# Performance work log

Measured on AMD Instinct MI355X. Metric: run time of the kernel, lower is better.

The kernel has to match this reference:

```python
import jax, jax.numpy as jnp
import numpy as np

B, T, I = 32, 512, 1024
H, HS = 8, 128  # n_heads, head_size; hidden = H*HS = 1024
LIM = 1.0 / np.sqrt(HS)


def setup_inputs() -> dict:
    key = jax.random.key(0)
    kx, kif, kzo, khh, kb = jax.random.split(key, 5)
    u = lambda k, shp: jax.random.uniform(k, shp, jnp.float32, -LIM, LIM)
    return {
        "xs": jax.random.normal(kx, (B, T, I), jnp.float32),
        "weight_if": u(kif, (H, 2 * HS, I)),
        "weight_zo": u(kzo, (H, 2 * HS, I)),
        "weight_hh": u(khh, (H, 4 * HS, HS)),
        "bias": u(kb, (H, 4 * HS)),
    }


def reference(xs, weight_if, weight_zo, weight_hh, bias):
    # xs: [B, T, I]. Scan the sLSTM cell over time, batched over B via einsum.
    b, t, _ = xs.shape
    n_heads, four_hs, head_size = weight_hh.shape

    def step(state, x):  # x: [B, I]
        h, c, m, n = state  # each [B, H, HS]
        if_lin = jnp.einsum('hki,bi->bhk', weight_if, x)  # [B, H, 2*HS]
        zo_lin = jnp.einsum('hki,bi->bhk', weight_zo, x)  # [B, H, 2*HS]
        lin = jnp.concatenate([if_lin, zo_lin], axis=2)
        lin = lin + jnp.einsum('hkd,bhd->bhk', weight_hh, h) + bias  # [B, H, 4*HS]
        i, f, z, o = jnp.split(lin, 4, axis=2)
        z = jnp.tanh(z)
        o = jax.nn.sigmoid(o)
        m_new = jnp.maximum(f + m, i)          # stabilizer
        i_e = jnp.exp(i - m_new)
        f_e = jnp.exp(f + m - m_new)
        c_new = f_e * c + i_e * z
        n_new = f_e * n + i_e
        h_new = o * (c_new / n_new)
        return (h_new, c_new, m_new, n_new), h_new.reshape(b, n_heads * head_size)

    init = tuple(jnp.zeros((b, n_heads, head_size), xs.dtype) for _ in range(4))
    _, hs = jax.lax.scan(step, init, jnp.swapaxes(xs, 0, 1))  # hs: [T, B, hidden]
    return jnp.swapaxes(hs, 0, 1)  # [B, T, hidden]
```

## Files before the change

kernel.cpp:

```cpp
#include <hip/hip_runtime.h>
#include <hip/hip_bf16.h>
#include <stdint.h>

#define B_SZ 32
#define T_SZ 512
#define I_SZ 1024
#define H_SZ 8
#define HS_SZ 128

typedef __attribute__((ext_vector_type(8))) short short8;
typedef __attribute__((ext_vector_type(4))) float f32x4;

static __device__ __forceinline__ unsigned short f2bf(float f) {
  union { float f; unsigned int u; } c; c.f = f;
  unsigned int u = c.u;
  unsigned int r = (u + 0x7fffu + ((u >> 16) & 1u)) >> 16;
  return (unsigned short)r;
}
static __device__ __forceinline__ float bf2f(unsigned short s) {
  union { unsigned int u; float f; } c; c.u = ((unsigned int)s) << 16;
  return c.f;
}
static __device__ __forceinline__ void split2(float x, unsigned short& hi,
                                              unsigned short& lo) {
  hi = f2bf(x);
  lo = f2bf(x - bf2f(hi));
}

__global__ void conv_x_split(const float* __restrict__ x,
                             unsigned short* __restrict__ ohi,
                             unsigned short* __restrict__ olo, int n4) {
  int i = blockIdx.x * blockDim.x + threadIdx.x;
  if (i >= n4) return;
  float4 v = ((const float4*)x)[i];
  ushort4 h, l;
  split2(v.x, h.x, l.x);
  split2(v.y, h.y, l.y);
  split2(v.z, h.z, l.z);
  split2(v.w, h.w, l.w);
  ((ushort4*)ohi)[i] = h;
  ((ushort4*)olo)[i] = l;
}

__global__ void conv_w_split(const float* __restrict__ wif,
                             const float* __restrict__ wzo,
                             unsigned short* __restrict__ ohi,
                             unsigned short* __restrict__ olo) {
  int i = blockIdx.x * blockDim.x + threadIdx.x;
  int flat = i * 4;
  int n = flat >> 10;
  int col = flat & 1023;
  int h = n >> 9, k4 = n & 511;
  const float* src = (k4 < 256)
                         ? (wif + ((size_t)(h * 256 + k4) * 1024 + col))
                         : (wzo + ((size_t)(h * 256 + (k4 - 256)) * 1024 + col));
  float4 v = *(const float4*)src;
  ushort4 hh, ll;
  split2(v.x, hh.x, ll.x);
  split2(v.y, hh.y, ll.y);
  split2(v.z, hh.z, ll.z);
  split2(v.w, hh.w, ll.w);
  ((ushort4*)ohi)[i] = hh;
  ((ushort4*)olo)[i] = ll;
}

__device__ __forceinline__ void gld_lds16(const void* g, void* l) {
  __builtin_amdgcn_global_load_lds(
      (const __attribute__((address_space(1))) void*)g,
      (__attribute__((address_space(3))) void*)l, 16, 0, 0);
}

__global__ __launch_bounds__(512)
void gemm3_kernel(const unsigned short* __restrict__ Ahi,
                  const unsigned short* __restrict__ Alo,
                  const unsigned short* __restrict__ Whi,
                  const unsigned short* __restrict__ Wlo,
                  float* __restrict__ G, int t0, int toff, int S, int lw) {
  __shared__ short lds2[2][32768];

  const int tid = threadIdx.x;
  const int lane = tid & 63, wv = tid >> 6;
  const int wm = wv >> 2, wn = wv & 3;
  const int bx = blockIdx.x, by = blockIdx.y;
  const int l15 = lane & 15, kg = lane >> 4;
  const int wmask = (1 << lw) - 1;

  const unsigned short* gsrc[8];
  int ldst[8];
#pragma unroll
  for (int t = 0; t < 4; ++t)
#pragma unroll
    for (int k = 0; k < 2; ++k) {
      int u = k * 512 + tid;
      int r = u >> 2, j = u & 3;
      int gslot = j ^ ((r >> 1) & 3);
      if (t < 2) {
        int cr = bx * 256 + r;
        size_t xsrow = (size_t)(cr >> lw) * 512 + t0 + (cr & wmask);
        gsrc[t * 2 + k] = ((t == 0) ? Ahi : Alo) + xsrow * 1024 + gslot * 8;
      } else {
        size_t wr = (size_t)by * 256 + r;
        gsrc[t * 2 + k] = ((t == 2) ? Whi : Wlo) + wr * 1024 + gslot * 8;
      }
      ldst[t * 2 + k] = t * 8192 + (k * 512 + wv * 64) * 8;
    }

  int offa[8], offw[4];
#pragma unroll
  for (int mi = 0; mi < 8; ++mi) {
    int r = wm * 128 + mi * 16 + l15;
    offa[mi] = r * 32 + (kg ^ ((r >> 1) & 3)) * 8;
  }
#pragma unroll
  for (int ni = 0; ni < 4; ++ni) {
    int r = wn * 64 + ni * 16 + l15;
    offw[ni] = r * 32 + (kg ^ ((r >> 1) & 3)) * 8;
  }

  f32x4 zero4 = {0.f, 0.f, 0.f, 0.f};
  f32x4 acc[8][4];
#pragma unroll
  for (int mi = 0; mi < 8; ++mi)
#pragma unroll
    for (int ni = 0; ni < 4; ++ni) acc[mi][ni] = zero4;

#pragma unroll
  for (int s8 = 0; s8 < 8; ++s8) gld_lds16(gsrc[s8], &lds2[0][ldst[s8]]);
#pragma unroll
  for (int s8 = 0; s8 < 8; ++s8)
    gld_lds16(gsrc[s8] + 32, &lds2[1][ldst[s8]]);
  asm volatile("s_waitcnt vmcnt(8)" : : : "memory");
  __builtin_amdgcn_s_barrier();

  for (int ks = 0; ks < 32; ++ks) {
    const short* bp = &lds2[ks & 1][0];

    short8 ah[8], wh4[4], wl4[4];
#pragma unroll
    for (int mi = 0; mi < 8; ++mi) ah[mi] = *(const short8*)(bp + offa[mi]);
#pragma unroll
    for (int ni = 0; ni < 4; ++ni)
      wh4[ni] = *(const short8*)(bp + 16384 + offw[ni]);

    __builtin_amdgcn_s_setprio(1);
#pragma unroll
    for (int mi = 0; mi < 8; ++mi)
#pragma unroll
      for (int ni = 0; ni < 4; ++ni)
        acc[mi][ni] = __builtin_amdgcn_mfma_f32_16x16x32_bf16(
            ah[mi], wh4[ni], acc[mi][ni], 0, 0, 0);
#pragma unroll
    for (int mi = 0; mi < 8; ++mi) {
      short8 al = *(const short8*)(bp + 8192 + offa[mi]);
#pragma unroll
      for (int ni = 0; ni < 4; ++ni)
        acc[mi][ni] = __builtin_amdgcn_mfma_f32_16x16x32_bf16(
            al, wh4[ni], acc[mi][ni], 0, 0, 0);
    }
#pragma unroll
    for (int ni = 0; ni < 4; ++ni)
      wl4[ni] = *(const short8*)(bp + 24576 + offw[ni]);
#pragma unroll
    for (int mi = 0; mi < 8; ++mi)
#pragma unroll
      for (int ni = 0; ni < 4; ++ni)
        acc[mi][ni] = __builtin_amdgcn_mfma_f32_16x16x32_bf16(
            ah[mi], wl4[ni], acc[mi][ni], 0, 0, 0);
    __builtin_amdgcn_s_setprio(0);

    asm volatile("s_waitcnt lgkmcnt(0)" : : : "memory");
    __builtin_amdgcn_sched_barrier(0);
    __builtin_amdgcn_s_barrier();

    if (ks + 2 < 32) {
#pragma unroll
      for (int s8 = 0; s8 < 8; ++s8)
        gld_lds16(gsrc[s8] + (ks + 2) * 32, &lds2[ks & 1][ldst[s8]]);
      asm volatile("s_waitcnt vmcnt(8)" : : : "memory");
    } else {
      asm volatile("s_waitcnt vmcnt(0)" : : : "memory");
    }
    __builtin_amdgcn_s_barrier();
  }

#pragma unroll
  for (int mi = 0; mi < 8; ++mi)
#pragma unroll
    for (int ni = 0; ni < 4; ++ni)
#pragma unroll
      for (int r = 0; r < 4; ++r) {
        int cr = bx * 256 + wm * 128 + mi * 16 + kg * 4 + r;
        int b = cr >> lw, m = cr & wmask;
        size_t growo = (size_t)b * S + toff + m;
        int gcol = by * 256 + wn * 64 + ni * 16 + l15;
        G[growo * 4096 + gcol] = acc[mi][ni][r];
      }
}

__global__ __launch_bounds__(512, 1)
void recur_kernel(const float* __restrict__ G,
                  const float* __restrict__ Whh,
                  const float* __restrict__ bias,
                  float* __restrict__ out,
                  float* __restrict__ state,
                  int t0, int tch, int first) {
  int blk = blockIdx.x;
  int b = blk >> 3, h = blk & 7;
  int t = threadIdx.x;
  int w = t >> 6;
  int l = t & 63;
  int q = w >> 1;
  int em = (w & 1) * 64 + l;
  int eg = q * 32 + (l & 31);

  __shared__ __align__(16) float part[2][128 * 20];

  float wreg[128];
  {
    const float* wb = Whh + (size_t)h * 65536 + (size_t)q * 32;
#pragma unroll
    for (int g = 0; g < 4; ++g) {
      const float4* wp = (const float4*)(wb + (size_t)(g * 128 + em) * 128);
#pragma unroll
      for (int c4 = 0; c4 < 8; ++c4) {
        float4 v = wp[c4];
        wreg[g * 32 + c4 * 4 + 0] = v.x;
        wreg[g * 32 + c4 * 4 + 1] = v.y;
        wreg[g * 32 + c4 * 4 + 2] = v.z;
        wreg[g * 32 + c4 * 4 + 3] = v.w;
      }
    }
  }
#pragma unroll
  for (int i = 0; i < 128; ++i)
    asm volatile("" : "+v"(wreg[i]));

  int si = (b * 8 + h) * 128 + eg;
  float hreg = 0.f, c_r = 0.f, n_r = 0.f, m_r = 0.f;
  if (!first) {
    hreg = state[si];
    c_r = state[32768 + si];
    m_r = state[65536 + si];
    n_r = state[98304 + si];
  }
  float bj0 = bias[h * 512 + eg];
  float bj1 = bias[h * 512 + 128 + eg];
  float bj2 = bias[h * 512 + 256 + eg];
  float bj3 = bias[h * 512 + 384 + eg];

  const float* gpb = G + (size_t)(b * tch) * 4096 + h * 512 + eg;
  float* op = out + ((size_t)b * 512 + t0) * 1024 + h * 128 + eg;
  bool writer = ((w & 1) == 0) && (l < 32);

  int ebase = em * 20 + q * 4;
  int rb0 = eg * 20 + 0;
  int rb1 = eg * 20 + 4;
  int rb2 = eg * 20 + 8;
  int rb3 = eg * 20 + 12;

  float g0 = gpb[0], g1 = gpb[128], g2 = gpb[256], g3 = gpb[384];

  for (int s = 0; s < tch; ++s) {
    float gn0 = 0.f, gn1 = 0.f, gn2 = 0.f, gn3 = 0.f;
    if (s + 1 < tch) {
      const float* gr = gpb + (size_t)(s + 1) * 4096;
      gn0 = gr[0]; gn1 = gr[128]; gn2 = gr[256]; gn3 = gr[384];
    }

    float a0 = 0.f, a1 = 0.f, a2 = 0.f, a3 = 0.f;
    int hbits = __float_as_int(hreg);
#pragma unroll
    for (int c = 0; c < 32; ++c) {
      float hs = __int_as_float(__builtin_amdgcn_readlane(hbits, c));
      a0 = fmaf(wreg[c], hs, a0);
      a1 = fmaf(wreg[32 + c], hs, a1);
      a2 = fmaf(wreg[64 + c], hs, a2);
      a3 = fmaf(wreg[96 + c], hs, a3);
    }
    float4 pv = {a0, a1, a2, a3};
    *(float4*)&part[s & 1][ebase] = pv;

    asm volatile("s_waitcnt lgkmcnt(0)" : : : "memory");
    __builtin_amdgcn_sched_barrier(0);
    __builtin_amdgcn_s_barrier();

    float4 p0 = *(const float4*)&part[s & 1][rb0];
    float4 p1 = *(const float4*)&part[s & 1][rb1];
    float4 p2 = *(const float4*)&part[s & 1][rb2];
    float4 p3 = *(const float4*)&part[s & 1][rb3];
    float iv = bj0 + g0 + ((p0.x + p1.x) + (p2.x + p3.x));
    float fv = bj1 + g1 + ((p0.y + p1.y) + (p2.y + p3.y));
    float zv = bj2 + g2 + ((p0.z + p1.z) + (p2.z + p3.z));
    float ov = bj3 + g3 + ((p0.w + p1.w) + (p2.w + p3.w));
    float e2 = __expf(2.f * zv);
    float zt = 1.f - 2.f * __builtin_amdgcn_rcpf(e2 + 1.f);
    float og = __builtin_amdgcn_rcpf(1.f + __expf(-ov));
    float mn = fmaxf(fv + m_r, iv);
    float ie = __expf(iv - mn);
    float fe = __expf(fv + m_r - mn);
    c_r = fe * c_r + ie * zt;
    n_r = fe * n_r + ie;
    m_r = mn;
    float hnew = og * c_r * __builtin_amdgcn_rcpf(n_r);
    hreg = hnew;
    if (writer) op[(size_t)s * 1024] = hnew;
    g0 = gn0; g1 = gn1; g2 = gn2; g3 = gn3;
  }

  if (writer) {
    state[si] = hreg;
    state[32768 + si] = c_r;
    state[65536 + si] = m_r;
    state[98304 + si] = n_r;
  }
}

extern "C" void kernel_launch(void* const* d_in, const int* in_sizes, int n_in,
                              void* d_out, int out_size, void* d_ws, size_t ws_size,
                              hipStream_t stream) {
  const float* xs   = (const float*)d_in[0];
  const float* wif  = (const float*)d_in[1];
  const float* wzo  = (const float*)d_in[2];
  const float* whh  = (const float*)d_in[3];
  const float* bias = (const float*)d_in[4];
  float* out = (float*)d_out;

  char* ws = (char*)d_ws;
  unsigned short* Ahi = (unsigned short*)ws;
  unsigned short* Alo = (unsigned short*)(ws + 33554432);
  unsigned short* Whi = (unsigned short*)(ws + 67108864);
  unsigned short* Wlo = (unsigned short*)(ws + 75497472);
  const size_t gbase = 83886080;

  int S = 256;
  while (S > 8 && gbase + (size_t)32 * S * 4096 * 4 + 524288 > ws_size)
    S >>= 1;
  int W = (S < 128) ? S : 128;
  int lw = 0;
  while ((1 << (lw + 1)) <= W) ++lw;

  float* G = (float*)(ws + gbase);
  float* state = (float*)(ws + gbase + (size_t)32 * S * 4096 * 4);

  conv_x_split<<<16384, 256, 0, stream>>>(xs, Ahi, Alo, 4194304);
  conv_w_split<<<4096, 256, 0, stream>>>(wif, wzo, Whi, Wlo);

  for (int t0 = 0; t0 < 512; t0 += S) {
    for (int tw = 0; tw < S; tw += W)
      gemm3_kernel<<<dim3((32 * W) / 256, 16), 512, 0, stream>>>(
          Ahi, Alo, Whi, Wlo, G, t0 + tw, tw, S, lw);
    recur_kernel<<<256, 512, 0, stream>>>(G, whh, bias, out, state, t0, S,
                                          t0 == 0);
  }
}
```

Baseline: 756.2 us.

## Merge conversion kernels, interleave A-fragment loads, fold gate inputs into partials

The two fp32-to-bf16 hi/lo split kernels are merged into one launch, saving one kernel launch. In the GEMM, the loads of the A high fragments are interleaved with the first MFMA group instead of all being issued up front, which may shorten the stall before the matrix work starts. In the recurrence, only the q==0 waves load the G and bias values and add them into their partial sums before the LDS reduction. This takes the per-step G loads and bias adds off most threads, and the sched_barrier is removed so the compiler has more freedom to schedule.

```diff
diff --git a/kernel.cpp b/kernel.cpp
--- a/kernel.cpp
+++ b/kernel.cpp
@@ -27,41 +27,42 @@
   lo = f2bf(x - bf2f(hi));
 }
 
-__global__ void conv_x_split(const float* __restrict__ x,
-                             unsigned short* __restrict__ ohi,
-                             unsigned short* __restrict__ olo, int n4) {
-  int i = blockIdx.x * blockDim.x + threadIdx.x;
-  if (i >= n4) return;
-  float4 v = ((const float4*)x)[i];
-  ushort4 h, l;
-  split2(v.x, h.x, l.x);
-  split2(v.y, h.y, l.y);
-  split2(v.z, h.z, l.z);
-  split2(v.w, h.w, l.w);
-  ((ushort4*)ohi)[i] = h;
-  ((ushort4*)olo)[i] = l;
-}
-
-__global__ void conv_w_split(const float* __restrict__ wif,
-                             const float* __restrict__ wzo,
-                             unsigned short* __restrict__ ohi,
-                             unsigned short* __restrict__ olo) {
-  int i = blockIdx.x * blockDim.x + threadIdx.x;
-  int flat = i * 4;
-  int n = flat >> 10;
-  int col = flat & 1023;
-  int h = n >> 9, k4 = n & 511;
-  const float* src = (k4 < 256)
-                         ? (wif + ((size_t)(h * 256 + k4) * 1024 + col))
-                         : (wzo + ((size_t)(h * 256 + (k4 - 256)) * 1024 + col));
-  float4 v = *(const float4*)src;
-  ushort4 hh, ll;
-  split2(v.x, hh.x, ll.x);
-  split2(v.y, hh.y, ll.y);
-  split2(v.z, hh.z, ll.z);
-  split2(v.w, hh.w, ll.w);
-  ((ushort4*)ohi)[i] = hh;
-  ((ushort4*)olo)[i] = ll;
+__global__ void conv_all(const float* __restrict__ x,
+                         const float* __restrict__ wif,
+                         const float* __restrict__ wzo,
+                         unsigned short* __restrict__ xhi,
+                         unsigned short* __restrict__ xlo,
+                         unsigned short* __restrict__ whi,
+                         unsigned short* __restrict__ wlo) {
+  int bid = blockIdx.x;
+  if (bid < 16384) {
+    int i = bid * 256 + threadIdx.x;
+    float4 v = ((const float4*)x)[i];
+    ushort4 h, l;
+    split2(v.x, h.x, l.x);
+    split2(v.y, h.y, l.y);
+    split2(v.z, h.z, l.z);
+    split2(v.w, h.w, l.w);
+    ((ushort4*)xhi)[i] = h;
+    ((ushort4*)xlo)[i] = l;
+  } else {
+    int i = (bid - 16384) * 256 + threadIdx.x;
+    int flat = i * 4;
+    int n = flat >> 10;
+    int col = flat & 1023;
+    int h = n >> 9, k4 = n & 511;
+    const float* src =
+        (k4 < 256) ? (wif + ((size_t)(h * 256 + k4) * 1024 + col))
+                   : (wzo + ((size_t)(h * 256 + (k4 - 256)) * 1024 + col));
+    float4 v = *(const float4*)src;
+    ushort4 hh, ll;
+    split2(v.x, hh.x, ll.x);
+    split2(v.y, hh.y, ll.y);
+    split2(v.z, hh.z, ll.z);
+    split2(v.w, hh.w, ll.w);
+    ((ushort4*)whi)[i] = hh;
+    ((ushort4*)wlo)[i] = ll;
+  }
 }
 
 __device__ __forceinline__ void gld_lds16(const void* g, void* l) {
@@ -137,18 +138,18 @@
 
     short8 ah[8], wh4[4], wl4[4];
 #pragma unroll
-    for (int mi = 0; mi < 8; ++mi) ah[mi] = *(const short8*)(bp + offa[mi]);
-#pragma unroll
     for (int ni = 0; ni < 4; ++ni)
       wh4[ni] = *(const short8*)(bp + 16384 + offw[ni]);
 
     __builtin_amdgcn_s_setprio(1);
 #pragma unroll
-    for (int mi = 0; mi < 8; ++mi)
+    for (int mi = 0; mi < 8; ++mi) {
+      ah[mi] = *(const short8*)(bp + offa[mi]);
 #pragma unroll
       for (int ni = 0; ni < 4; ++ni)
         acc[mi][ni] = __builtin_amdgcn_mfma_f32_16x16x32_bf16(
             ah[mi], wh4[ni], acc[mi][ni], 0, 0, 0);
+    }
 #pragma unroll
     for (int mi = 0; mi < 8; ++mi) {
       short8 al = *(const short8*)(bp + 8192 + offa[mi]);
@@ -212,6 +213,7 @@
   int q = w >> 1;
   int em = (w & 1) * 64 + l;
   int eg = q * 32 + (l & 31);
+  bool gq0 = (q == 0);
 
   __shared__ __align__(16) float part[2][128 * 20];
 
@@ -243,12 +245,21 @@
     m_r = state[65536 + si];
     n_r = state[98304 + si];
   }
-  float bj0 = bias[h * 512 + eg];
-  float bj1 = bias[h * 512 + 128 + eg];
-  float bj2 = bias[h * 512 + 256 + eg];
-  float bj3 = bias[h * 512 + 384 + eg];
-
-  const float* gpb = G + (size_t)(b * tch) * 4096 + h * 512 + eg;
+
+  float bm0 = 0.f, bm1 = 0.f, bm2 = 0.f, bm3 = 0.f;
+  float g0 = 0.f, g1 = 0.f, g2 = 0.f, g3 = 0.f;
+  const float* gpm = G + (size_t)(b * tch) * 4096 + h * 512 + em;
+  if (gq0) {
+    bm0 = bias[h * 512 + em];
+    bm1 = bias[h * 512 + 128 + em];
+    bm2 = bias[h * 512 + 256 + em];
+    bm3 = bias[h * 512 + 384 + em];
+    g0 = gpm[0];
+    g1 = gpm[128];
+    g2 = gpm[256];
+    g3 = gpm[384];
+  }
+
   float* op = out + ((size_t)b * 512 + t0) * 1024 + h * 128 + eg;
   bool writer = ((w & 1) == 0) && (l < 32);
 
@@ -258,12 +269,10 @@
   int rb2 = eg * 20 + 8;
   int rb3 = eg * 20 + 12;
 
-  float g0 = gpb[0], g1 = gpb[128], g2 = gpb[256], g3 = gpb[384];
-
   for (int s = 0; s < tch; ++s) {
     float gn0 = 0.f, gn1 = 0.f, gn2 = 0.f, gn3 = 0.f;
-    if (s + 1 < tch) {
-      const float* gr = gpb + (size_t)(s + 1) * 4096;
+    if (gq0 && s + 1 < tch) {
+      const float* gr = gpm + (size_t)(s + 1) * 4096;
       gn0 = gr[0]; gn1 = gr[128]; gn2 = gr[256]; gn3 = gr[384];
     }
 
@@ -277,21 +286,26 @@
       a2 = fmaf(wreg[64 + c], hs, a2);
       a3 = fmaf(wreg[96 + c], hs, a3);
     }
+    if (gq0) {
+      a0 += bm0 + g0;
+      a1 += bm1 + g1;
+      a2 += bm2 + g2;
+      a3 += bm3 + g3;
+    }
     float4 pv = {a0, a1, a2, a3};
     *(float4*)&part[s & 1][ebase] = pv;
 
     asm volatile("s_waitcnt lgkmcnt(0)" : : : "memory");
-    __builtin_amdgcn_sched_barrier(0);
     __builtin_amdgcn_s_barrier();
 
     float4 p0 = *(const float4*)&part[s & 1][rb0];
     float4 p1 = *(const float4*)&part[s & 1][rb1];
     float4 p2 = *(const float4*)&part[s & 1][rb2];
     float4 p3 = *(const float4*)&part[s & 1][rb3];
-    float iv = bj0 + g0 + ((p0.x + p1.x) + (p2.x + p3.x));
-    float fv = bj1 + g1 + ((p0.y + p1.y) + (p2.y + p3.y));
-    float zv = bj2 + g2 + ((p0.z + p1.z) + (p2.z + p3.z));
-    float ov = bj3 + g3 + ((p0.w + p1.w) + (p2.w + p3.w));
+    float iv = (p0.x + p1.x) + (p2.x + p3.x);
+    float fv = (p0.y + p1.y) + (p2.y + p3.y);
+    float zv = (p0.z + p1.z) + (p2.z + p3.z);
+    float ov = (p0.w + p1.w) + (p2.w + p3.w);
     float e2 = __expf(2.f * zv);
     float zt = 1.f - 2.f * __builtin_amdgcn_rcpf(e2 + 1.f);
     float og = __builtin_amdgcn_rcpf(1.f + __expf(-ov));
@@ -304,7 +318,7 @@
     float hnew = og * c_r * __builtin_amdgcn_rcpf(n_r);
     hreg = hnew;
     if (writer) op[(size_t)s * 1024] = hnew;
-    g0 = gn0; g1 = gn1; g2 = gn2; g3 = gn3;
+    if (gq0) { g0 = gn0; g1 = gn1; g2 = gn2; g3 = gn3; }
   }
 
   if (writer) {
@@ -342,8 +356,7 @@
   float* G = (float*)(ws + gbase);
   float* state = (float*)(ws + gbase + (size_t)32 * S * 4096 * 4);
 
-  conv_x_split<<<16384, 256, 0, stream>>>(xs, Ahi, Alo, 4194304);
-  conv_w_split<<<4096, 256, 0, stream>>>(wif, wzo, Whi, Wlo);
+  conv_all<<<20480, 256, 0, stream>>>(xs, wif, wzo, Ahi, Alo, Whi, Wlo);
 
   for (int t0 = 0; t0 < 512; t0 += S) {
     for (int tw = 0; tw < S; tw += W)
```

New measurement: 763.0 us. No clear change (+0.9%).
